# Optimization experiments

Hardware: AMD Instinct MI355X
Metric: run time of the kernel (lower is better)

The kernel has to match this reference:

```python
import jax, jax.numpy as jnp
import numpy as np

H_IMG, W_IMG = 60, 80          # hardcoded grid in get_positional_encodings
NUM_HEADS = 8
DIM = 256
N_TOK = H_IMG * W_IMG          # 4800

# Hardcoded intrinsics in the source: fx=517/9, fy=517/8, cx=40, cy=30.
# fx_norm = fx/(2*cx)*2, fy_norm = fy/(2*cy)*2 ; cx_norm = cy_norm = 0,
# so Kinv is diagonal and Kinv @ [x, y, 1] = [x/fx_n, y/fy_n, 1].
_FX_N = (517.0 / 9.0) / 80.0 * 2.0
_FY_N = (517.0 / 8.0) / 60.0 * 2.0


def _positional(B):
    ys = jnp.linspace(-1.0, 1.0, H_IMG)
    xs = jnp.linspace(-1.0, 1.0, W_IMG)
    # loop index j*w + k: y varies over rows (outer), x over cols (inner)
    p3 = jnp.repeat(ys, W_IMG) / _FY_N   # (N,) = y'/w'
    p4 = jnp.tile(xs, H_IMG) / _FX_N     # (N,) = x'/w'
    pos = jnp.stack([p3 * p3, p4 * p4, p3 * p4, p3, p4, jnp.ones_like(p3)], axis=-1)  # (N,6)
    return jnp.broadcast_to(pos, (B, N_TOK, 6))


def setup_inputs() -> dict:
    key = jax.random.key(0)
    k1, k2, k3, k4, k5 = jax.random.split(key, 5)
    B, N, C, H = 1, N_TOK, DIM, NUM_HEADS
    return {
        "x1": jax.random.normal(k1, (B, N, C), dtype=jnp.float32),
        "x2": jax.random.normal(k2, (B, N, C), dtype=jnp.float32),
        "qkv_w": jax.random.normal(k3, (3 * C, C), dtype=jnp.float32) * 0.02,
        "proj_w": jax.random.normal(k4, (C, C + 6 * H), dtype=jnp.float32) * 0.02,
        "proj_b": jax.random.normal(k5, (C,), dtype=jnp.float32) * 0.02,
    }


def reference(x1, x2, qkv_w, proj_w, proj_b):
    B, N, C = x1.shape
    H = NUM_HEADS
    hd = C // H
    scale = hd ** -0.5
    D = hd + 6

    def qkv(x):
        y = (x @ qkv_w.T).reshape(B, N, 3, H, hd).transpose(2, 0, 3, 1, 4)
        return y[0], y[1], y[2]   # each (B,H,N,hd)

    q1, k1, v1 = qkv(x1)
    q2, k2, v2 = qkv(x2)

    pos_h = jnp.broadcast_to(_positional(B)[:, None], (B, H, N, 6))

    def fundamental(q, k, v):
        a = jnp.einsum('bhnd,bhmd->bhnm', q, k) * scale          # (B,H,N,N)
        af = jax.nn.softmax(a, axis=-1) * jax.nn.softmax(a, axis=-2)  # dual softmax
        vc = jnp.concatenate([v, pos_h], axis=-1)                 # (B,H,N,D)
        f = jnp.einsum('bhnc,bhnm->bhcm', vc, af)                 # V^T A
        f = jnp.einsum('bhcm,bhmd->bhcd', f, vc)                  # (V^T A) V -> (B,H,D,D)
        f = f.reshape(B, H * D, D).transpose(0, 2, 1)             # (B, D, H*D)
        return f @ proj_w.T + proj_b                              # (B, D, C)

    fundamental_1 = fundamental(q2, k1, v1)
    fundamental_2 = fundamental(q1, k2, v2)
    return fundamental_2, fundamental_1
```

## Files before the change

### kernel.cpp

```cpp
#include <hip/hip_runtime.h>
#include <stdint.h>
#include <math.h>

#define N_TOK 4800
#define NH 8
#define HD 32
#define DP 40
#define DD 38
#define NTILES 150
#define MCHUNK 3
#define FRAG 2048
#define SCALE 0.17677669529663687f
#define QSCALE (0.17677669529663687f * 1.4426950408889634f)

typedef float f32x16 __attribute__((ext_vector_type(16)));
typedef float f32x2 __attribute__((ext_vector_type(2)));
typedef short s8v __attribute__((ext_vector_type(8)));
typedef int i2v __attribute__((ext_vector_type(2)));

#if __has_builtin(__builtin_amdgcn_exp2f)
#define EXP2F(x) __builtin_amdgcn_exp2f(x)
#else
#define EXP2F(x) exp2f(x)
#endif

__device__ __forceinline__ unsigned short f2bf(float x) {
    union { float f; uint32_t u; } v; v.f = x;
    uint32_t r = v.u + 0x7FFFu + ((v.u >> 16) & 1u);
    return (unsigned short)(r >> 16);
}
__device__ __forceinline__ float bf2f(unsigned short h) {
    union { uint32_t u; float f; } v; v.u = ((uint32_t)h) << 16;
    return v.f;
}
__device__ __forceinline__ int cvtpk(float lo, float hi) {
    int r;
    asm("v_cvt_pk_bf16_f32 %0, %1, %2" : "=v"(r) : "v"(lo), "v"(hi));
    return r;
}
__device__ __forceinline__ s8v mk_s8(int a, int b, int c, int d) {
    union { int i[4]; s8v s; } u;
    u.i[0] = a; u.i[1] = b; u.i[2] = c; u.i[3] = d;
    return u.s;
}
__device__ __forceinline__ float posv(int m, int idx) {
    const int rrow = m / 80, rcol = m % 80;
    const float y = -1.0f + (float)rrow * (2.0f / 59.0f);
    const float x = -1.0f + (float)rcol * (2.0f / 79.0f);
    const float p3 = y * (240.0f / 517.0f);
    const float p4 = x * (360.0f / 517.0f);
    if (idx == 0) return p3 * p3;
    if (idx == 1) return p4 * p4;
    if (idx == 2) return p3 * p4;
    if (idx == 3) return p3;
    if (idx == 4) return p4;
    return 1.0f;
}

template<int NX, int NY, int NZ>
__device__ __forceinline__ void swzdec(int& x, int& y, int& z) {
    const int L = blockIdx.x + NX * (blockIdx.y + NY * blockIdx.z);
    constexpr int cpx = NX * NY * NZ / 8;
    const int s = (L & 7) * cpx + (L >> 3);
    x = s % NX;
    const int r = s / NX;
    y = r % NY;
    z = r / NY;
}
template<int NX, int NY, int NZ>
__device__ __forceinline__ void swzdec_xo(int& x, int& y, int& z) {
    const int L = blockIdx.x + NX * (blockIdx.y + NY * blockIdx.z);
    constexpr int cpx = NX * NY * NZ / 8;
    const int s = (L & 7) * cpx + (L >> 3);
    x = s / (NY * NZ);
    const int r = s % (NY * NZ);
    y = r % NY;
    z = r / NY;
}

#define MFMA(a, b, c) __builtin_amdgcn_mfma_f32_32x32x16_bf16((a), (b), (c), 0, 0, 0)

__global__ __launch_bounds__(256) void frag_kernel(
    const float* __restrict__ x1, unsigned short* __restrict__ xh1,
    const float* __restrict__ x2, unsigned short* __restrict__ xh2,
    const float* __restrict__ w, unsigned short* __restrict__ wh,
    float* __restrict__ zbase, int zn4)
{
    int b = blockIdx.x;
    const int t = threadIdx.x;
    if (b >= 324) {
        const int i = (b - 324) * 256 + t;
        if (i < zn4) ((float4*)zbase)[i] = make_float4(0.f, 0.f, 0.f, 0.f);
        return;
    }
    const float* src; unsigned short* dh;
    if (b < 150)      { src = x1 + b * 8192; dh = xh1 + b * 8192; }
    else if (b < 300) { b -= 150; src = x2 + b * 8192; dh = xh2 + b * 8192; }
    else              { b -= 300; src = w + b * 8192; dh = wh + b * 8192; }
#pragma unroll
    for (int k = 0; k < 4; ++k) {
        const int f = k * 256 + t;
        const int c = f >> 6;
        const int rem = f & 63;
        const float* sp = src + (rem & 31) * 256 + c * 16 + (rem >> 5) * 8;
        const float4 a = *(const float4*)(sp);
        const float4 bb = *(const float4*)(sp + 4);
        const float vv[8] = {a.x, a.y, a.z, a.w, bb.x, bb.y, bb.z, bb.w};
        union { unsigned short s[8]; s8v v; } H;
#pragma unroll
        for (int j = 0; j < 8; ++j) H.s[j] = f2bf(vv[j]);
        *(s8v*)(dh + f * 8) = H.v;
    }
}

__global__ __launch_bounds__(128, 4) void qkv_mfma_kernel(
    const unsigned short* __restrict__ xhA, unsigned short* __restrict__ qbA,
    unsigned short* __restrict__ kbA, float* __restrict__ vcbA,
    const unsigned short* __restrict__ xhB, unsigned short* __restrict__ qbB,
    unsigned short* __restrict__ kbB, float* __restrict__ vcbB,
    const unsigned short* __restrict__ wh)
{
    __shared__ float tlbuf[2][32][33];
    int bx, by, bz;
    swzdec_xo<75, 12, 2>(bx, by, bz);
    const int sel = bz;
    const unsigned short* xh = sel ? xhB : xhA;
    unsigned short* qb = sel ? qbB : qbA;
    unsigned short* kb = sel ? kbB : kbA;
    float* vcb = sel ? vcbB : vcbA;
    const int lane = threadIdx.x & 63;
    const int wid = threadIdx.x >> 6;
    const int xtile = bx * 2 + wid;
    const unsigned short* xp = xh + (size_t)xtile * 8192 + lane * 8;
    const unsigned short* wp0 = wh + (size_t)(by * 2) * 8192 + lane * 8;
    const unsigned short* wp1 = wp0 + 8192;
    f32x16 acc0 = {}, acc1 = {};
#pragma unroll
    for (int c = 0; c < 16; ++c) {
        const s8v aH = *(const s8v*)(xp + c * 512);
        const s8v b0 = *(const s8v*)(wp0 + c * 512);
        const s8v b1 = *(const s8v*)(wp1 + c * 512);
        acc0 = MFMA(aH, b0, acc0);
        acc1 = MFMA(aH, b1, acc1);
    }
    const int lr = lane & 31, hi5 = lane >> 5;
    const int row = lane >> 1, ch = (lane & 1) * 16;
    float (*T)[33] = tlbuf[wid];
#pragma unroll
    for (int jj = 0; jj < 2; ++jj) {
#pragma unroll
        for (int r = 0; r < 16; ++r) {
            const float v = jj ? acc1[r] : acc0[r];
            T[(r & 3) + 8 * (r >> 2) + 4 * hi5][lr] = v;
        }
        const int jt = by * 2 + jj, s = jt >> 3, h = jt & 7;
        const int n = xtile * 32 + row;
        if (s == 2) {
            float4* dst = (float4*)&vcb[(size_t)(h * N_TOK + n) * HD + ch];
#pragma unroll
            for (int k = 0; k < 4; ++k) {
                dst[k] = make_float4(T[row][ch + 4 * k + 0], T[row][ch + 4 * k + 1],
                                     T[row][ch + 4 * k + 2], T[row][ch + 4 * k + 3]);
            }
        } else {
            const float m = (s == 0) ? QSCALE : 1.0f;
            unsigned short* dst = (s == 0 ? qb : kb)
                                  + (size_t)(h * N_TOK + n) * HD + ch;
            union { unsigned short u[8]; s8v v; } o0, o1;
#pragma unroll
            for (int i = 0; i < 8; ++i) {
                o0.u[i] = f2bf(T[row][ch + i] * m);
                o1.u[i] = f2bf(T[row][ch + 8 + i] * m);
            }
            *(s8v*)dst = o0.v;
            *(s8v*)(dst + 8) = o1.v;
        }
    }
}

__global__ __launch_bounds__(192, 4) void cs_kernel(
    const unsigned short* __restrict__ qbA, const unsigned short* __restrict__ kbA,
    float* __restrict__ csA,
    const unsigned short* __restrict__ qbB, const unsigned short* __restrict__ kbB,
    float* __restrict__ csB)
{
    int bx, by, bz;
    swzdec<25, 5, 16>(bx, by, bz);
    const int sel = bz >> 3;
    const unsigned short* qb = sel ? qbB : qbA;
    const unsigned short* kb = sel ? kbB : kbA;
    float* cs = sel ? csB : csA;
    const int lane = threadIdx.x & 63;
    const int wid = threadIdx.x >> 6;
    const int h = bz & 7;
    const int m0 = bx * 192 + wid * 64;
    const int lr = lane & 31, hi5 = lane >> 5;
    const int hbase = h * N_TOK;
    const unsigned short* kp = kb + (hbase + m0 + lr) * HD + 8 * hi5;
    const s8v bK0 = *(const s8v*)(kp);
    const s8v bK1 = *(const s8v*)(kp + 16);
    const s8v bK2 = *(const s8v*)(kp + 32 * HD);
    const s8v bK3 = *(const s8v*)(kp + 32 * HD + 16);
    const unsigned short* qp = qb + (hbase + by * 960 + lr) * HD + 8 * hi5;
    s8v qa0[2], qa1[2];
    qa0[0] = *(const s8v*)(qp);
    qa1[0] = *(const s8v*)(qp + 16);
    qp += 32 * HD;
    qa0[1] = *(const s8v*)(qp);
    qa1[1] = *(const s8v*)(qp + 16);
    qp += 32 * HD;
    f32x2 cA0 = {0.f, 0.f}, cA1 = {0.f, 0.f};
    f32x2 cB0 = {0.f, 0.f}, cB1 = {0.f, 0.f};
#pragma unroll 2
    for (int it = 0; it < 30; ++it) {
        const int c = it & 1;
        f32x16 accA = {}, accB = {};
        accA = MFMA(qa0[c], bK0, accA);
        accB = MFMA(qa0[c], bK2, accB);
        accA = MFMA(qa1[c], bK1, accA);
        accB = MFMA(qa1[c], bK3, accB);
#pragma unroll
        for (int k = 0; k < 8; ++k) {
            f32x2 eA, eB;
            eA.x = EXP2F(accA[2 * k]);
            eA.y = EXP2F(accA[2 * k + 1]);
            eB.x = EXP2F(accB[2 * k]);
            eB.y = EXP2F(accB[2 * k + 1]);
            if (k & 1) { cA1 += eA; cB1 += eB; }
            else       { cA0 += eA; cB0 += eB; }
        }
        qa0[c] = *(const s8v*)(qp);
        qa1[c] = *(const s8v*)(qp + 16);
        qp += 32 * HD;
    }
    float cA = cA0.x + cA0.y + cA1.x + cA1.y;
    float cB = cB0.x + cB0.y + cB1.x + cB1.y;
    cA += __shfl_xor(cA, 32);
    cB += __shfl_xor(cB, 32);
    if (lane < 32) {
        atomicAdd(&cs[hbase + m0 + lane], cA);
        atomicAdd(&cs[hbase + m0 + 32 + lane], cB);
    }
}

__global__ __launch_bounds__(256) void vfrag_kernel(
    const float* __restrict__ vcA, const float* __restrict__ csA,
    unsigned short* __restrict__ vfA,
    const float* __restrict__ vcB, const float* __restrict__ csB,
    unsigned short* __restrict__ vfB)
{
    const int sel = blockIdx.y >> 3;
    const float* vc = sel ? vcB : vcA;
    const float* cs = sel ? csB : csA;
    unsigned short* vf = sel ? vfB : vfA;
    __shared__ float vl[32][33];
    __shared__ float ul[32];
    const int mt = blockIdx.x;
    const int h = blockIdx.y & 7;
    const int t = threadIdx.x;
    const int m0 = mt * 32;
    const float* vcbase = vc + (size_t)(h * N_TOK + m0) * HD;
    for (int e = t; e < 32 * HD; e += 256) vl[e >> 5][e & 31] = vcbase[e];
    if (t < 32) ul[t] = 1.0f / cs[(size_t)h * N_TOK + m0 + t];
    __syncthreads();
    const int b = t >> 6, lane = t & 63;
    const int hi5 = lane >> 5, lr = lane & 31;
    const int d = (b >> 1) * 32 + lr;
    const int mb = (b & 1) * 16 + hi5 * 8;
    union { unsigned short s[8]; s8v v; } pk;
#pragma unroll
    for (int j = 0; j < 8; ++j) {
        const int mo = mb + j;
        float v;
        if (d < 32)      v = vl[mo][d];
        else if (d < 38) v = posv(m0 + mo, d - 32);
        else             v = 0.0f;
        pk.s[j] = f2bf(v * ul[mo]);
    }
    *(s8v*)(vf + ((size_t)(h * NTILES + mt) * 4 + b) * 512 + lane * 8) = pk.v;
}

__global__ __launch_bounds__(192, 4) void tprime_mfma_kernel(
    const unsigned short* __restrict__ qbA, const unsigned short* __restrict__ kbA,
    const unsigned short* __restrict__ vfA, float* __restrict__ rsA,
    unsigned short* __restrict__ TA0, unsigned short* __restrict__ TA1,
    unsigned short* __restrict__ TA2,
    const unsigned short* __restrict__ qbB, const unsigned short* __restrict__ kbB,
    const unsigned short* __restrict__ vfB, float* __restrict__ rsB,
    unsigned short* __restrict__ TB0, unsigned short* __restrict__ TB1,
    unsigned short* __restrict__ TB2)
{
    int bx, by, bz;
    swzdec<50, MCHUNK, 16>(bx, by, bz);
    const int sel = bz >> 3;
    const unsigned short* qb = sel ? qbB : qbA;
    const unsigned short* kb = sel ? kbB : kbA;
    const unsigned short* vf = sel ? vfB : vfA;
    float* rs = sel ? rsB : rsA;
    unsigned short* T = sel ? (by == 0 ? TB0 : (by == 1 ? TB1 : TB2))
                            : (by == 0 ? TA0 : (by == 1 ? TA1 : TA2));
    const int lane = threadIdx.x & 63;
    const int wid = threadIdx.x >> 6;
    const int h = bz & 7;
    const int n0 = bx * 96 + wid * 32;
    const int lr = lane & 31, hi5 = lane >> 5;
    const int hbase = h * N_TOK;
    const unsigned short* qp = qb + (hbase + n0 + lr) * HD + 8 * hi5;
    const s8v bQ0 = *(const s8v*)(qp);
    const s8v bQ1 = *(const s8v*)(qp + 16);
    f32x16 t0 = {}, t1 = {};
    const int mt0 = by * 50;
    const unsigned short* kp = kb + (hbase + mt0 * 32 + lr) * HD + 8 * hi5;
    const unsigned short* vp = vf + (size_t)(h * NTILES + mt0) * FRAG + lane * 8;
    s8v a0[2], a1[2], v00[2], v01[2], v10[2], v11[2];
#pragma unroll
    for (int j = 0; j < 2; ++j) {
        a0[j] = *(const s8v*)(kp);
        a1[j] = *(const s8v*)(kp + 16);
        v00[j] = *(const s8v*)(vp);
        v01[j] = *(const s8v*)(vp + 512);
        v10[j] = *(const s8v*)(vp + 1024);
        v11[j] = *(const s8v*)(vp + 1536);
        kp += 32 * HD;
        vp += FRAG;
    }
    f32x2 rsa = {0.f, 0.f}, rsb = {0.f, 0.f};
#pragma unroll 2
    for (int it = 0; it < 50; ++it) {
        const int c = it & 1;
        f32x16 s = {};
        s = MFMA(a0[c], bQ0, s);
        s = MFMA(a1[c], bQ1, s);
        f32x2 p2[8];
#pragma unroll
        for (int k = 0; k < 8; ++k) {
            f32x2 e2;
            e2.x = EXP2F(s[2 * k]);
            e2.y = EXP2F(s[2 * k + 1]);
            if (k & 1) rsb += e2; else rsa += e2;
            p2[k] = e2 * e2;
        }
        const int L0 = cvtpk(p2[0].x, p2[0].y), L1 = cvtpk(p2[1].x, p2[1].y);
        const int H0 = cvtpk(p2[2].x, p2[2].y), H1 = cvtpk(p2[3].x, p2[3].y);
        const int L2 = cvtpk(p2[4].x, p2[4].y), L3 = cvtpk(p2[5].x, p2[5].y);
        const int H2 = cvtpk(p2[6].x, p2[6].y), H3 = cvtpk(p2[7].x, p2[7].y);
        const i2v s0 = __builtin_amdgcn_permlane32_swap(L0, H0, false, false);
        const i2v s1 = __builtin_amdgcn_permlane32_swap(L1, H1, false, false);
        const i2v s2 = __builtin_amdgcn_permlane32_swap(L2, H2, false, false);
        const i2v s3 = __builtin_amdgcn_permlane32_swap(L3, H3, false, false);
        const s8v pa0 = mk_s8(s0[0], s1[0], s0[1], s1[1]);
        const s8v pa1 = mk_s8(s2[0], s3[0], s2[1], s3[1]);
        __builtin_amdgcn_s_setprio(1);
        t0 = MFMA(pa0, v00[c], t0);
        t0 = MFMA(pa1, v01[c], t0);
        t1 = MFMA(pa0, v10[c], t1);
        t1 = MFMA(pa1, v11[c], t1);
        __builtin_amdgcn_s_setprio(0);
        a0[c] = *(const s8v*)(kp);
        a1[c] = *(const s8v*)(kp + 16);
        v00[c] = *(const s8v*)(vp);
        v01[c] = *(const s8v*)(vp + 512);
        v10[c] = *(const s8v*)(vp + 1024);
        v11[c] = *(const s8v*)(vp + 1536);
        kp += 32 * HD;
        vp += FRAG;
    }
    float rsacc = rsa.x + rsa.y + rsb.x + rsb.y;
    rsacc += __shfl_xor(rsacc, 32);
    if (lane < 32) atomicAdd(&rs[hbase + n0 + lane], rsacc);
    unsigned int* Tw = (unsigned int*)T;
#pragma unroll
    for (int r = 0; r < 16; ++r) {
        const int n = n0 + (r & 3) + 8 * (r >> 2) + 4 * hi5;
        const float par0 = __shfl_xor(t0[r], 1);
        const float par1 = __shfl_xor(t1[r], 1);
        if (!(lr & 1)) {
            Tw[(size_t)(hbase + n) * (DP / 2) + (lr >> 1)] =
                (unsigned int)cvtpk(t0[r], par0);
            if (lr < 8)
                Tw[(size_t)(hbase + n) * (DP / 2) + 16 + (lr >> 1)] =
                    (unsigned int)cvtpk(t1[r], par1);
        }
    }
}

__global__ __launch_bounds__(256) void fgemm_kernel(
    const float* __restrict__ VCA, const float* __restrict__ rsA,
    const unsigned short* __restrict__ TA0, const unsigned short* __restrict__ TA1,
    const unsigned short* __restrict__ TA2, float* __restrict__ fA,
    const float* __restrict__ VCB, const float* __restrict__ rsB,
    const unsigned short* __restrict__ TB0, const unsigned short* __restrict__ TB1,
    const unsigned short* __restrict__ TB2, float* __restrict__ fB)
{
    const int sel = blockIdx.x >> 3;
    const float* VC = sel ? VCB : VCA;
    const float* rs = sel ? rsB : rsA;
    const unsigned short* Ta = sel ? TB0 : TA0;
    const unsigned short* Tb = sel ? TB1 : TA1;
    const unsigned short* Tc = sel ? TB2 : TA2;
    float* f = sel ? fB : fA;
    __shared__ __align__(16) float wvcl[64 * DP];
    __shared__ __align__(16) float tl[64 * DP];
    __shared__ float wl[64];
    const int h = blockIdx.x & 7, n0 = blockIdx.y * 64;
    const int t = threadIdx.x;
    if (t < 64) wl[t] = 1.0f / rs[(size_t)h * N_TOK + n0 + t];
    __syncthreads();
    const float* vcbase = VC + (size_t)(h * N_TOK + n0) * HD;
    const ushort4* ta4 = (const ushort4*)(Ta + (size_t)(h * N_TOK + n0) * DP);
    const ushort4* tb4 = (const ushort4*)(Tb + (size_t)(h * N_TOK + n0) * DP);
    const ushort4* tc4 = (const ushort4*)(Tc + (size_t)(h * N_TOK + n0) * DP);
    for (int e4 = t; e4 < 64 * DP / 4; e4 += 256) {
        const ushort4 a4 = ta4[e4];
        const ushort4 b4 = tb4[e4];
        const ushort4 c4 = tc4[e4];
        tl[e4 * 4 + 0] = bf2f(a4.x) + bf2f(b4.x) + bf2f(c4.x);
        tl[e4 * 4 + 1] = bf2f(a4.y) + bf2f(b4.y) + bf2f(c4.y);
        tl[e4 * 4 + 2] = bf2f(a4.z) + bf2f(b4.z) + bf2f(c4.z);
        tl[e4 * 4 + 3] = bf2f(a4.w) + bf2f(b4.w) + bf2f(c4.w);
    }
    for (int e = t; e < 64 * DP; e += 256) {
        const int row = e / DP, c = e - row * DP;
        float v;
        if (c < 32)      v = vcbase[row * HD + c];
        else if (c < 38) v = posv(n0 + row, c - 32);
        else             v = 0.0f;
        wvcl[e] = v * wl[row];
    }
    __syncthreads();
    for (int p = t; p < DD * DD; p += 256) {
        const int c = p / DD, d = p % DD;
        float s = 0.f;
#pragma unroll 8
        for (int n = 0; n < 64; ++n) s += wvcl[n * DP + c] * tl[n * DP + d];
        atomicAdd(&f[(size_t)(h * DD + c) * DP + d], s);
    }
}

__global__ __launch_bounds__(256) void out_kernel(
    const float* __restrict__ f1, const float* __restrict__ f2,
    const float* __restrict__ pw, const float* __restrict__ pb,
    float* __restrict__ out)
{
    const int sel = blockIdx.y;
    const float* f = sel ? f2 : f1;
    float* dst = sel ? out : (out + DD * 256);
    __shared__ __align__(16) float flds[304];
    const int d = blockIdx.x, t = threadIdx.x;
    for (int j = t; j < 304; j += 256) flds[j] = f[(size_t)j * DP + d];
    __syncthreads();
    float acc = pb[t];
    const float* pwrow = pw + (size_t)t * 304;
#pragma unroll 4
    for (int j = 0; j < 304; j += 4) {
        const float4 p4 = *(const float4*)&pwrow[j];
        const float4 f4 = *(const float4*)&flds[j];
        acc += p4.x * f4.x + p4.y * f4.y + p4.z * f4.z + p4.w * f4.w;
    }
    dst[(size_t)d * 256 + t] = acc;
}

extern "C" void kernel_launch(void* const* d_in, const int* in_sizes, int n_in,
                              void* d_out, int out_size, void* d_ws, size_t ws_size,
                              hipStream_t stream)
{
    const float* x1 = (const float*)d_in[0];
    const float* x2 = (const float*)d_in[1];
    const float* qkv_w = (const float*)d_in[2];
    const float* proj_w = (const float*)d_in[3];
    const float* proj_b = (const float*)d_in[4];
    float* out = (float*)d_out;

    const size_t QSZ = (size_t)NH * N_TOK * HD;
    const size_t VSZ = (size_t)NH * N_TOK * DP;
    const size_t SSZ = (size_t)NH * N_TOK;
    const size_t FSZ = (size_t)NH * DD * DP;
    const size_t XSZ = (size_t)N_TOK * 256;
    const size_t WSZ = (size_t)768 * 256;
    const size_t VTSZ = (size_t)NH * NTILES * FRAG;

    float* vc1 = (float*)d_ws;
    float* vc2 = vc1 + QSZ;
    float* rs1 = vc2 + QSZ;
    float* cs1 = rs1 + SSZ;
    float* rs2 = cs1 + SSZ;
    float* cs2 = rs2 + SSZ;
    float* f1 = cs2 + SSZ;
    float* f2 = f1 + FSZ;
    unsigned short* xh1 = (unsigned short*)(f2 + FSZ);
    unsigned short* xh2 = xh1 + XSZ;
    unsigned short* wh = xh2 + XSZ;
    unsigned short* qb1 = wh + WSZ;
    unsigned short* kb1 = qb1 + QSZ;
    unsigned short* qb2 = kb1 + QSZ;
    unsigned short* kb2 = qb2 + QSZ;
    unsigned short* vf1 = kb2 + QSZ;
    unsigned short* vf2 = vf1 + VTSZ;
    unsigned short* T1a = vf2 + VTSZ;
    unsigned short* T1b = T1a + VSZ;
    unsigned short* T1c = T1b + VSZ;
    unsigned short* T2a = T1c + VSZ;
    unsigned short* T2b = T2a + VSZ;
    unsigned short* T2c = T2b + VSZ;

    const int zn4 = (int)((4 * SSZ + 2 * FSZ) / 4);

    frag_kernel<<<324 + 174, 256, 0, stream>>>(x1, xh1, x2, xh2, qkv_w, wh,
                                               rs1, zn4);

    qkv_mfma_kernel<<<dim3(75, 12, 2), 128, 0, stream>>>(
        xh1, qb1, kb1, vc1, xh2, qb2, kb2, vc2, wh);

    cs_kernel<<<dim3(25, 5, 16), 192, 0, stream>>>(qb2, kb1, cs1,
                                                   qb1, kb2, cs2);
    vfrag_kernel<<<dim3(150, 16), 256, 0, stream>>>(vc1, cs1, vf1,
                                                    vc2, cs2, vf2);
    tprime_mfma_kernel<<<dim3(50, MCHUNK, 16), 192, 0, stream>>>(
        qb2, kb1, vf1, rs1, T1a, T1b, T1c,
        qb1, kb2, vf2, rs2, T2a, T2b, T2c);
    fgemm_kernel<<<dim3(16, 75), 256, 0, stream>>>(
        vc1, rs1, T1a, T1b, T1c, f1,
        vc2, rs2, T2a, T2b, T2c, f2);
    out_kernel<<<dim3(38, 2), 256, 0, stream>>>(f1, f2, proj_w, proj_b, out);
}
```

Measured before the change: 211.9 us.

## Process two query tiles per wave in tprime kernel to reuse K/V fragments

Each wave now handles 64 query rows (two 32-row MFMA tiles) instead of 32, sharing every loaded K and V fragment between both tiles, and the grid's x dimension is halved. This halves global K/V fragment traffic per query and gives two independent exp/MFMA chains for latency hiding. In exchange it doubles accumulator registers, lowers the occupancy target to 3 blocks, and replaces the two-deep register prefetch with a single-step prefetch.

After: 334.7 us. 57.9% more time.

```diff
diff --git a/kernel.cpp b/kernel.cpp
--- a/kernel.cpp
+++ b/kernel.cpp
@@ -280,7 +280,7 @@
     *(s8v*)(vf + ((size_t)(h * NTILES + mt) * 4 + b) * 512 + lane * 8) = pk.v;
 }
 
-__global__ __launch_bounds__(192, 4) void tprime_mfma_kernel(
+__global__ __launch_bounds__(192, 3) void tprime_mfma_kernel(
     const unsigned short* __restrict__ qbA, const unsigned short* __restrict__ kbA,
     const unsigned short* __restrict__ vfA, float* __restrict__ rsA,
     unsigned short* __restrict__ TA0, unsigned short* __restrict__ TA1,
@@ -291,7 +291,7 @@
     unsigned short* __restrict__ TB2)
 {
     int bx, by, bz;
-    swzdec<50, MCHUNK, 16>(bx, by, bz);
+    swzdec<25, MCHUNK, 16>(bx, by, bz);
     const int sel = bz >> 3;
     const unsigned short* qb = sel ? qbB : qbA;
     const unsigned short* kb = sel ? kbB : kbA;
@@ -302,84 +302,125 @@
     const int lane = threadIdx.x & 63;
     const int wid = threadIdx.x >> 6;
     const int h = bz & 7;
-    const int n0 = bx * 96 + wid * 32;
+    const int n0 = bx * 192 + wid * 64;
     const int lr = lane & 31, hi5 = lane >> 5;
     const int hbase = h * N_TOK;
     const unsigned short* qp = qb + (hbase + n0 + lr) * HD + 8 * hi5;
     const s8v bQ0 = *(const s8v*)(qp);
     const s8v bQ1 = *(const s8v*)(qp + 16);
-    f32x16 t0 = {}, t1 = {};
+    const s8v bQ2 = *(const s8v*)(qp + 32 * HD);
+    const s8v bQ3 = *(const s8v*)(qp + 32 * HD + 16);
+    f32x16 t0A = {}, t1A = {}, t0B = {}, t1B = {};
     const int mt0 = by * 50;
     const unsigned short* kp = kb + (hbase + mt0 * 32 + lr) * HD + 8 * hi5;
     const unsigned short* vp = vf + (size_t)(h * NTILES + mt0) * FRAG + lane * 8;
-    s8v a0[2], a1[2], v00[2], v01[2], v10[2], v11[2];
-#pragma unroll
-    for (int j = 0; j < 2; ++j) {
-        a0[j] = *(const s8v*)(kp);
-        a1[j] = *(const s8v*)(kp + 16);
-        v00[j] = *(const s8v*)(vp);
-        v01[j] = *(const s8v*)(vp + 512);
-        v10[j] = *(const s8v*)(vp + 1024);
-        v11[j] = *(const s8v*)(vp + 1536);
-        kp += 32 * HD;
-        vp += FRAG;
-    }
-    f32x2 rsa = {0.f, 0.f}, rsb = {0.f, 0.f};
+    s8v a0 = *(const s8v*)(kp);
+    s8v a1 = *(const s8v*)(kp + 16);
+    s8v v00 = *(const s8v*)(vp);
+    s8v v01 = *(const s8v*)(vp + 512);
+    s8v v10 = *(const s8v*)(vp + 1024);
+    s8v v11 = *(const s8v*)(vp + 1536);
+    f32x2 rsA0 = {0.f, 0.f}, rsA1 = {0.f, 0.f};
+    f32x2 rsB0 = {0.f, 0.f}, rsB1 = {0.f, 0.f};
 #pragma unroll 2
     for (int it = 0; it < 50; ++it) {
-        const int c = it & 1;
-        f32x16 s = {};
-        s = MFMA(a0[c], bQ0, s);
-        s = MFMA(a1[c], bQ1, s);
-        f32x2 p2[8];
-#pragma unroll
-        for (int k = 0; k < 8; ++k) {
-            f32x2 e2;
-            e2.x = EXP2F(s[2 * k]);
-            e2.y = EXP2F(s[2 * k + 1]);
-            if (k & 1) rsb += e2; else rsa += e2;
-            p2[k] = e2 * e2;
+        kp += 32 * HD; vp += FRAG;
+        const s8v na0 = *(const s8v*)(kp);
+        const s8v na1 = *(const s8v*)(kp + 16);
+        const s8v nv00 = *(const s8v*)(vp);
+        const s8v nv01 = *(const s8v*)(vp + 512);
+        const s8v nv10 = *(const s8v*)(vp + 1024);
+        const s8v nv11 = *(const s8v*)(vp + 1536);
+        f32x16 sA = {}, sB = {};
+        sA = MFMA(a0, bQ0, sA);
+        sB = MFMA(a0, bQ2, sB);
+        sA = MFMA(a1, bQ1, sA);
+        sB = MFMA(a1, bQ3, sB);
+        {
+            f32x2 p2[8];
+#pragma unroll
+            for (int k = 0; k < 8; ++k) {
+                f32x2 e2;
+                e2.x = EXP2F(sA[2 * k]);
+                e2.y = EXP2F(sA[2 * k + 1]);
+                if (k & 1) rsA1 += e2; else rsA0 += e2;
+                p2[k] = e2 * e2;
+            }
+            const int L0 = cvtpk(p2[0].x, p2[0].y), L1 = cvtpk(p2[1].x, p2[1].y);
+            const int H0 = cvtpk(p2[2].x, p2[2].y), H1 = cvtpk(p2[3].x, p2[3].y);
+            const int L2 = cvtpk(p2[4].x, p2[4].y), L3 = cvtpk(p2[5].x, p2[5].y);
+            const int H2 = cvtpk(p2[6].x, p2[6].y), H3 = cvtpk(p2[7].x, p2[7].y);
+            const i2v s0 = __builtin_amdgcn_permlane32_swap(L0, H0, false, false);
+            const i2v s1 = __builtin_amdgcn_permlane32_swap(L1, H1, false, false);
+            const i2v s2 = __builtin_amdgcn_permlane32_swap(L2, H2, false, false);
+            const i2v s3 = __builtin_amdgcn_permlane32_swap(L3, H3, false, false);
+            const s8v pa0 = mk_s8(s0[0], s1[0], s0[1], s1[1]);
+            const s8v pa1 = mk_s8(s2[0], s3[0], s2[1], s3[1]);
+            __builtin_amdgcn_s_setprio(1);
+            t0A = MFMA(pa0, v00, t0A);
+            t0A = MFMA(pa1, v01, t0A);
+            t1A = MFMA(pa0, v10, t1A);
+            t1A = MFMA(pa1, v11, t1A);
+            __builtin_amdgcn_s_setprio(0);
         }
-        const int L0 = cvtpk(p2[0].x, p2[0].y), L1 = cvtpk(p2[1].x, p2[1].y);
-        const int H0 = cvtpk(p2[2].x, p2[2].y), H1 = cvtpk(p2[3].x, p2[3].y);
-        const int L2 = cvtpk(p2[4].x, p2[4].y), L3 = cvtpk(p2[5].x, p2[5].y);
-        const int H2 = cvtpk(p2[6].x, p2[6].y), H3 = cvtpk(p2[7].x, p2[7].y);
-        const i2v s0 = __builtin_amdgcn_permlane32_swap(L0, H0, false, false);
-        const i2v s1 = __builtin_amdgcn_permlane32_swap(L1, H1, false, false);
-        const i2v s2 = __builtin_amdgcn_permlane32_swap(L2, H2, false, false);
-        const i2v s3 = __builtin_amdgcn_permlane32_swap(L3, H3, false, false);
-        const s8v pa0 = mk_s8(s0[0], s1[0], s0[1], s1[1]);
-        const s8v pa1 = mk_s8(s2[0], s3[0], s2[1], s3[1]);
-        __builtin_amdgcn_s_setprio(1);
-        t0 = MFMA(pa0, v00[c], t0);
-        t0 = MFMA(pa1, v01[c], t0);
-        t1 = MFMA(pa0, v10[c], t1);
-        t1 = MFMA(pa1, v11[c], t1);
-        __builtin_amdgcn_s_setprio(0);
-        a0[c] = *(const s8v*)(kp);
-        a1[c] = *(const s8v*)(kp + 16);
-        v00[c] = *(const s8v*)(vp);
-        v01[c] = *(const s8v*)(vp + 512);
-        v10[c] = *(const s8v*)(vp + 1024);
-        v11[c] = *(const s8v*)(vp + 1536);
-        kp += 32 * HD;
-        vp += FRAG;
-    }
-    float rsacc = rsa.x + rsa.y + rsb.x + rsb.y;
-    rsacc += __shfl_xor(rsacc, 32);
-    if (lane < 32) atomicAdd(&rs[hbase + n0 + lane], rsacc);
+        {
+            f32x2 p2[8];
+#pragma unroll
+            for (int k = 0; k < 8; ++k) {
+                f32x2 e2;
+                e2.x = EXP2F(sB[2 * k]);
+                e2.y = EXP2F(sB[2 * k + 1]);
+                if (k & 1) rsB1 += e2; else rsB0 += e2;
+                p2[k] = e2 * e2;
+            }
+            const int L0 = cvtpk(p2[0].x, p2[0].y), L1 = cvtpk(p2[1].x, p2[1].y);
+            const int H0 = cvtpk(p2[2].x, p2[2].y), H1 = cvtpk(p2[3].x, p2[3].y);
+            const int L2 = cvtpk(p2[4].x, p2[4].y), L3 = cvtpk(p2[5].x, p2[5].y);
+            const int H2 = cvtpk(p2[6].x, p2[6].y), H3 = cvtpk(p2[7].x, p2[7].y);
+            const i2v s0 = __builtin_amdgcn_permlane32_swap(L0, H0, false, false);
+            const i2v s1 = __builtin_amdgcn_permlane32_swap(L1, H1, false, false);
+            const i2v s2 = __builtin_amdgcn_permlane32_swap(L2, H2, false, false);
+            const i2v s3 = __builtin_amdgcn_permlane32_swap(L3, H3, false, false);
+            const s8v pa0 = mk_s8(s0[0], s1[0], s0[1], s1[1]);
+            const s8v pa1 = mk_s8(s2[0], s3[0], s2[1], s3[1]);
+            __builtin_amdgcn_s_setprio(1);
+            t0B = MFMA(pa0, v00, t0B);
+            t0B = MFMA(pa1, v01, t0B);
+            t1B = MFMA(pa0, v10, t1B);
+            t1B = MFMA(pa1, v11, t1B);
+            __builtin_amdgcn_s_setprio(0);
+        }
+        a0 = na0; a1 = na1;
+        v00 = nv00; v01 = nv01; v10 = nv10; v11 = nv11;
+    }
+    float rA = rsA0.x + rsA0.y + rsA1.x + rsA1.y;
+    float rB = rsB0.x + rsB0.y + rsB1.x + rsB1.y;
+    rA += __shfl_xor(rA, 32);
+    rB += __shfl_xor(rB, 32);
+    if (lane < 32) {
+        atomicAdd(&rs[hbase + n0 + lane], rA);
+        atomicAdd(&rs[hbase + n0 + 32 + lane], rB);
+    }
     unsigned int* Tw = (unsigned int*)T;
 #pragma unroll
     for (int r = 0; r < 16; ++r) {
-        const int n = n0 + (r & 3) + 8 * (r >> 2) + 4 * hi5;
-        const float par0 = __shfl_xor(t0[r], 1);
-        const float par1 = __shfl_xor(t1[r], 1);
+        const int crow = (r & 3) + 8 * (r >> 2) + 4 * hi5;
+        const int nA = n0 + crow, nB = n0 + 32 + crow;
+        const float pA0 = __shfl_xor(t0A[r], 1);
+        const float pA1 = __shfl_xor(t1A[r], 1);
+        const float pB0 = __shfl_xor(t0B[r], 1);
+        const float pB1 = __shfl_xor(t1B[r], 1);
         if (!(lr & 1)) {
-            Tw[(size_t)(hbase + n) * (DP / 2) + (lr >> 1)] =
-                (unsigned int)cvtpk(t0[r], par0);
-            if (lr < 8)
-                Tw[(size_t)(hbase + n) * (DP / 2) + 16 + (lr >> 1)] =
-                    (unsigned int)cvtpk(t1[r], par1);
+            Tw[(size_t)(hbase + nA) * (DP / 2) + (lr >> 1)] =
+                (unsigned int)cvtpk(t0A[r], pA0);
+            Tw[(size_t)(hbase + nB) * (DP / 2) + (lr >> 1)] =
+                (unsigned int)cvtpk(t0B[r], pB0);
+            if (lr < 8) {
+                Tw[(size_t)(hbase + nA) * (DP / 2) + 16 + (lr >> 1)] =
+                    (unsigned int)cvtpk(t1A[r], pA1);
+                Tw[(size_t)(hbase + nB) * (DP / 2) + 16 + (lr >> 1)] =
+                    (unsigned int)cvtpk(t1B[r], pB1);
+            }
         }
     }
 }
@@ -515,7 +556,7 @@
                                                    qb1, kb2, cs2);
     vfrag_kernel<<<dim3(150, 16), 256, 0, stream>>>(vc1, cs1, vf1,
                                                     vc2, cs2, vf2);
-    tprime_mfma_kernel<<<dim3(50, MCHUNK, 16), 192, 0, stream>>>(
+    tprime_mfma_kernel<<<dim3(25, MCHUNK, 16), 192, 0, stream>>>(
         qb2, kb1, vf1, rs1, T1a, T1b, T1c,
         qb1, kb2, vf2, rs2, T2a, T2b, T2c);
     fgemm_kernel<<<dim3(16, 75), 256, 0, stream>>>(
```
